# Kernel tuning notes

Hardware: AMD Instinct MI355X
Metric: run time of the kernel (lower is better)

## Reference

```python
import jax, jax.numpy as jnp
import numpy as np

N_NODES = 50000
N_EDGES = 400000
IN_CH = 814
HID = 128
HEADS1 = 4
NUM_CLASSES = 46
NUM_GRAPHS = 64
NEG_SLOPE = 0.2


def setup_inputs() -> dict:
    key = jax.random.key(0)
    ks = jax.random.split(key, 16)
    x = jax.random.normal(ks[0], (N_NODES, IN_CH), dtype=jnp.float32)
    edge_index = jax.random.randint(ks[1], (2, N_EDGES), 0, N_NODES, dtype=jnp.int32)
    batch = jnp.sort(jax.random.randint(ks[2], (N_NODES,), 0, NUM_GRAPHS, dtype=jnp.int32))
    s = 0.05
    # GATConv 1: in 814 -> 4 heads x 128, concat
    W1 = jax.random.normal(ks[3], (IN_CH, HEADS1 * HID), dtype=jnp.float32) * s
    a_src1 = jax.random.normal(ks[4], (HEADS1, HID), dtype=jnp.float32) * s
    a_dst1 = jax.random.normal(ks[5], (HEADS1, HID), dtype=jnp.float32) * s
    b1 = jnp.zeros((HEADS1 * HID,), dtype=jnp.float32)
    # GATConv 2: in 512 -> 1 head x 128, no concat (mean)
    W2 = jax.random.normal(ks[6], (HEADS1 * HID, HID), dtype=jnp.float32) * s
    a_src2 = jax.random.normal(ks[7], (1, HID), dtype=jnp.float32) * s
    a_dst2 = jax.random.normal(ks[8], (1, HID), dtype=jnp.float32) * s
    b2 = jnp.zeros((HID,), dtype=jnp.float32)
    # MLP head 128 -> 64 -> 46 (dropout is identity in eval mode)
    fc1_w = jax.random.normal(ks[9], (HID, 64), dtype=jnp.float32) * s
    fc1_b = jnp.zeros((64,), dtype=jnp.float32)
    fc2_w = jax.random.normal(ks[10], (64, NUM_CLASSES), dtype=jnp.float32) * s
    fc2_b = jnp.zeros((NUM_CLASSES,), dtype=jnp.float32)
    return {"x": x, "edge_index": edge_index, "batch": batch,
            "W1": W1, "a_src1": a_src1, "a_dst1": a_dst1, "b1": b1,
            "W2": W2, "a_src2": a_src2, "a_dst2": a_dst2, "b2": b2,
            "fc1_w": fc1_w, "fc1_b": fc1_b, "fc2_w": fc2_w, "fc2_b": fc2_b}


def _gat_layer(x, src, dst, W, a_src, a_dst, bias, heads, out_ch, concat):
    # PyG GATConv: linear transform, edge attention w/ LeakyReLU,
    # segment softmax over destination nodes, scatter-add aggregation.
    n = x.shape[0]
    h = (x @ W).reshape(n, heads, out_ch)                 # [N,H,C]
    al_s = jnp.einsum('nhc,hc->nh', h, a_src)             # [N,H]
    al_d = jnp.einsum('nhc,hc->nh', h, a_dst)             # [N,H]
    e = jax.nn.leaky_relu(al_s[src] + al_d[dst], NEG_SLOPE)  # [E,H]
    m = jax.ops.segment_max(e, dst, num_segments=n)       # [N,H]
    ex = jnp.exp(e - m[dst])
    denom = jax.ops.segment_sum(ex, dst, num_segments=n)  # [N,H]
    alpha = ex / denom[dst]                               # [E,H]
    out = jax.ops.segment_sum(h[src] * alpha[:, :, None], dst, num_segments=n)  # [N,H,C]
    if concat:
        return out.reshape(n, heads * out_ch) + bias
    return out.mean(axis=1) + bias


def reference(x, edge_index, batch, W1, a_src1, a_dst1, b1,
              W2, a_src2, a_dst2, b2, fc1_w, fc1_b, fc2_w, fc2_b):
    n = x.shape[0]
    # GATConv adds self-loops by default
    loops = jnp.arange(n, dtype=edge_index.dtype)
    src = jnp.concatenate([edge_index[0], loops])
    dst = jnp.concatenate([edge_index[1], loops])
    h = jax.nn.relu(_gat_layer(x, src, dst, W1, a_src1, a_dst1, b1, HEADS1, HID, True))
    h = jax.nn.relu(_gat_layer(h, src, dst, W2, a_src2, a_dst2, b2, 1, HID, False))
    # global mean pool over graphs
    sums = jax.ops.segment_sum(h, batch, num_segments=NUM_GRAPHS)      # [G,128]
    cnts = jax.ops.segment_sum(jnp.ones((n,), h.dtype), batch, num_segments=NUM_GRAPHS)
    pooled = sums / jnp.maximum(cnts, 1.0)[:, None]
    # MLP head (dropout = identity at inference)
    z = jax.nn.relu(pooled @ fc1_w + fc1_b)
    return z @ fc2_w + fc2_b
```

## Files before the change

kernel.cpp:

```cpp
#include <hip/hip_runtime.h>
#include <hip/hip_bf16.h>

#define N_NODES 50000
#define N_EDGES 400000
#define IN_CH   814
#define HID     128
#define HEADS1  4
#define NUM_GRAPHS 64
#define NUM_CLASSES 46
#define NEG_SLOPE 0.2f
#define KP 832

typedef __attribute__((ext_vector_type(8))) short bf16x8;
typedef __attribute__((ext_vector_type(4))) float f32x4;

__device__ __forceinline__ float leaky(float v) { return v > 0.f ? v : NEG_SLOPE * v; }

__device__ __forceinline__ unsigned short f2bf(float f) {
  unsigned u = __float_as_uint(f);
  unsigned r = u + 0x7fff + ((u >> 16) & 1);
  return (unsigned short)(r >> 16);
}
__device__ __forceinline__ float bf2f(short s) {
  return __uint_as_float(((unsigned)(unsigned short)s) << 16);
}

#define GLOAD_LDS16(g, l)                                                        \
  __builtin_amdgcn_global_load_lds((const __attribute__((address_space(1))) unsigned*)(g), \
                                   (__attribute__((address_space(3))) unsigned*)(l), 16, 0, 0)

__global__ __launch_bounds__(256) void convert_x(const float* __restrict__ x,
                                                 unsigned short* __restrict__ Ab) {
  const int row = blockIdx.x;
  const int c = threadIdx.x * 4;
  if (c >= KP) return;
  const float* xr = x + (size_t)row * IN_CH;
  float v[4] = {0.f, 0.f, 0.f, 0.f};
  if (c + 3 < IN_CH) {
    float2 u0 = *(const float2*)(xr + c);
    float2 u1 = *(const float2*)(xr + c + 2);
    v[0] = u0.x; v[1] = u0.y; v[2] = u1.x; v[3] = u1.y;
  } else {
#pragma unroll
    for (int k = 0; k < 4; k++) if (c + k < IN_CH) v[k] = xr[c + k];
  }
  ushort4 o = make_ushort4(f2bf(v[0]), f2bf(v[1]), f2bf(v[2]), f2bf(v[3]));
  *(ushort4*)&Ab[(size_t)row * KP + c] = o;
}

__global__ __launch_bounds__(256) void convert_w1t(const float* __restrict__ W1,
                                                   unsigned short* __restrict__ Bt) {
  const int n = blockIdx.x;
  unsigned short* br = Bt + (size_t)n * KP;
  for (int k = threadIdx.x; k < KP; k += 256) {
    const float v = (k < IN_CH) ? W1[(size_t)k * 512 + n] : 0.f;
    br[k] = f2bf(v);
  }
}

__global__ __launch_bounds__(256) void convert_w2t(const float* __restrict__ W2,
                                                   unsigned short* __restrict__ Bt2) {
  const int n = blockIdx.x;
  unsigned short* br = Bt2 + (size_t)n * 512;
  for (int k = threadIdx.x; k < 512; k += 256) br[k] = f2bf(W2[(size_t)k * 128 + n]);
}

template<int KPITCH, int CPITCH, bool OUTBF>
__global__ __launch_bounds__(256) void gemm_mfma(const unsigned short* __restrict__ A,
                                                 const unsigned short* __restrict__ B,
                                                 void* __restrict__ Cv) {
  __shared__ unsigned short sA[8 * 128 * 8];
  __shared__ unsigned short sB[8 * 128 * 8];
  const int tid = threadIdx.x;
  const int w = tid >> 6, lane = tid & 63;
  const int row0 = blockIdx.x * 128;
  const int col0 = blockIdx.y * 128;
  const int wr = w >> 1, wc = w & 1;

  f32x4 acc[4][4];
#pragma unroll
  for (int mi = 0; mi < 4; mi++)
#pragma unroll
    for (int nj = 0; nj < 4; nj++) acc[mi][nj] = (f32x4){0.f, 0.f, 0.f, 0.f};

  long a_off[4], b_off[4];
  int lds_base[4];
#pragma unroll
  for (int c = 0; c < 4; c++) {
    const int s = (w * 4 + c) * 64 + lane;
    const int kg = s >> 7, r = s & 127;
    int arow = row0 + r; if (arow >= N_NODES) arow = N_NODES - 1;
    a_off[c] = (long)arow * KPITCH + kg * 8;
    b_off[c] = (long)(col0 + r) * KPITCH + kg * 8;
    lds_base[c] = (w * 4 + c) * 64 * 8;
  }
  int aoff[4][2], boff[4][2];
#pragma unroll
  for (int i = 0; i < 4; i++)
#pragma unroll
    for (int ks = 0; ks < 2; ks++) {
      aoff[i][ks] = ((ks * 4 + (lane >> 4)) * 128 + wr * 64 + i * 16 + (lane & 15)) * 8;
      boff[i][ks] = ((ks * 4 + (lane >> 4)) * 128 + wc * 64 + i * 16 + (lane & 15)) * 8;
    }

  for (int kt = 0; kt < KPITCH / 64; ++kt) {
    const int kbase = kt * 64;
#pragma unroll
    for (int c = 0; c < 4; c++) {
      GLOAD_LDS16(A + (a_off[c] + kbase), &sA[lds_base[c]]);
      GLOAD_LDS16(B + (b_off[c] + kbase), &sB[lds_base[c]]);
    }
    __syncthreads();
    bf16x8 af[4][2], bfr[4][2];
#pragma unroll
    for (int mi = 0; mi < 4; mi++)
#pragma unroll
      for (int ks = 0; ks < 2; ks++) af[mi][ks] = *(const bf16x8*)&sA[aoff[mi][ks]];
#pragma unroll
    for (int nj = 0; nj < 4; nj++)
#pragma unroll
      for (int ks = 0; ks < 2; ks++) bfr[nj][ks] = *(const bf16x8*)&sB[boff[nj][ks]];
#pragma unroll
    for (int mi = 0; mi < 4; mi++)
#pragma unroll
      for (int nj = 0; nj < 4; nj++) {
        acc[mi][nj] = __builtin_amdgcn_mfma_f32_16x16x32_bf16(af[mi][0], bfr[nj][0], acc[mi][nj], 0, 0, 0);
        acc[mi][nj] = __builtin_amdgcn_mfma_f32_16x16x32_bf16(af[mi][1], bfr[nj][1], acc[mi][nj], 0, 0, 0);
      }
    __syncthreads();
  }
  const int r4 = (lane >> 4) * 4;
  const int cc = lane & 15;
#pragma unroll
  for (int mi = 0; mi < 4; mi++) {
#pragma unroll
    for (int r = 0; r < 4; r++) {
      const int gr = row0 + wr * 64 + mi * 16 + r4 + r;
      if (gr < N_NODES) {
        if (OUTBF) {
          unsigned short* cp = (unsigned short*)Cv + (size_t)gr * CPITCH + col0 + wc * 64 + cc;
#pragma unroll
          for (int nj = 0; nj < 4; nj++) cp[nj * 16] = f2bf(acc[mi][nj][r]);
        } else {
          float* cp = (float*)Cv + (size_t)gr * CPITCH + col0 + wc * 64 + cc;
#pragma unroll
          for (int nj = 0; nj < 4; nj++) cp[nj * 16] = acc[mi][nj][r];
        }
      }
    }
  }
}

__global__ __launch_bounds__(256) void attn_prep1(const unsigned short* __restrict__ h1b,
                                                  const float* __restrict__ a_src,
                                                  const float* __restrict__ a_dst,
                                                  float* __restrict__ als,
                                                  float* __restrict__ ald) {
  const int n = blockIdx.x * 4 + (threadIdx.x >> 6);
  const int lane = threadIdx.x & 63;
  if (n >= N_NODES) return;
  const int c0 = lane * 8;
  const bf16x8 hv = *(const bf16x8*)&h1b[(size_t)n * 512 + c0];
  float ps = 0.f, pd = 0.f;
#pragma unroll
  for (int j = 0; j < 8; j++) {
    const float f = bf2f(hv[j]);
    ps += f * a_src[c0 + j];
    pd += f * a_dst[c0 + j];
  }
#pragma unroll
  for (int off = 8; off; off >>= 1) {
    ps += __shfl_xor(ps, off);
    pd += __shfl_xor(pd, off);
  }
  if ((lane & 15) == 0) {
    als[n * 4 + (lane >> 4)] = ps;
    ald[n * 4 + (lane >> 4)] = pd;
  }
}

__global__ __launch_bounds__(256) void attn_prep2(const float* __restrict__ h2,
                                                  const float* __restrict__ a_src,
                                                  const float* __restrict__ a_dst,
                                                  float* __restrict__ als,
                                                  float* __restrict__ ald) {
  const int n = blockIdx.x * 4 + (threadIdx.x >> 6);
  const int lane = threadIdx.x & 63;
  if (n >= N_NODES) return;
  const float* hr = h2 + (size_t)n * 128;
  float h0 = hr[lane], h1v = hr[lane + 64];
  float ps = h0 * a_src[lane] + h1v * a_src[lane + 64];
  float pd = h0 * a_dst[lane] + h1v * a_dst[lane + 64];
#pragma unroll
  for (int off = 32; off; off >>= 1) {
    ps += __shfl_xor(ps, off);
    pd += __shfl_xor(pd, off);
  }
  if (lane == 0) { als[n] = ps; ald[n] = pd; }
}

__global__ void init_misc(int* deg, float* pooled, float* cnts) {
  const int i = blockIdx.x * 256 + threadIdx.x;
  if (i < N_NODES) deg[i] = 1;
  if (i < NUM_GRAPHS * HID) pooled[i] = 0.f;
  if (i < NUM_GRAPHS) cnts[i] = 0.f;
}

__global__ void hist_kernel(const int* __restrict__ dst, int* deg) {
  const int e = blockIdx.x * 256 + threadIdx.x;
  if (e < N_EDGES) atomicAdd(&deg[dst[e]], 1);
}

__global__ __launch_bounds__(256) void scan_block_sum(const int* __restrict__ deg, int* bsum) {
  __shared__ int sd[256];
  const int t = threadIdx.x;
  const int i = blockIdx.x * 256 + t;
  sd[t] = (i < N_NODES) ? deg[i] : 0;
  __syncthreads();
  for (int s = 128; s; s >>= 1) { if (t < s) sd[t] += sd[t + s]; __syncthreads(); }
  if (t == 0) bsum[blockIdx.x] = sd[0];
}

__global__ __launch_bounds__(256) void scan_base(const int* __restrict__ bsum, int* bbase, int* offsets) {
  __shared__ int tmp[256];
  const int t = threadIdx.x;
  const int nb = (N_NODES + 255) / 256;
  const int v = (t < nb) ? bsum[t] : 0;
  tmp[t] = v;
  __syncthreads();
  for (int off = 1; off < 256; off <<= 1) {
    int a = (t >= off) ? tmp[t - off] : 0;
    __syncthreads();
    tmp[t] += a;
    __syncthreads();
  }
  if (t < nb) bbase[t] = tmp[t] - v;
  if (t == 255) offsets[N_NODES] = tmp[255];
}

__global__ __launch_bounds__(256) void scan_final(const int* __restrict__ deg,
                                                  const int* __restrict__ bbase,
                                                  int* offsets, int* cursor) {
  __shared__ int tmp[256];
  const int t = threadIdx.x;
  const int i = blockIdx.x * 256 + t;
  const int v = (i < N_NODES) ? deg[i] : 0;
  tmp[t] = v;
  __syncthreads();
  for (int off = 1; off < 256; off <<= 1) {
    int a = (t >= off) ? tmp[t - off] : 0;
    __syncthreads();
    tmp[t] += a;
    __syncthreads();
  }
  if (i < N_NODES) {
    const int excl = bbase[blockIdx.x] + tmp[t] - v;
    offsets[i] = excl;
    cursor[i] = excl;
  }
}

__global__ void scatter_kernel(const int* __restrict__ src, const int* __restrict__ dst,
                               int* cursor, int* __restrict__ srcs) {
  const int e = blockIdx.x * 256 + threadIdx.x;
  if (e >= N_EDGES + N_NODES) return;
  int s, d;
  if (e < N_EDGES) { s = src[e]; d = dst[e]; }
  else { s = e - N_EDGES; d = s; }
  const int p = atomicAdd(&cursor[d], 1);
  srcs[p] = s;
}

__global__ __launch_bounds__(256) void aggregate1(const unsigned short* __restrict__ h1b,
                                                  const float* __restrict__ als,
                                                  const float* __restrict__ ald,
                                                  const int* __restrict__ offsets,
                                                  const int* __restrict__ srcs,
                                                  const float* __restrict__ b1,
                                                  unsigned short* __restrict__ x2b) {
  const int n = blockIdx.x * 4 + (threadIdx.x >> 6);
  const int lane = threadIdx.x & 63;
  if (n >= N_NODES) return;
  const int beg = offsets[n], end = offsets[n + 1];
  const int h = lane >> 4;
  const int c0 = lane * 8;
  const float aldh = ald[n * 4 + h];
  float m = -1e30f;
  for (int p = beg; p < end; p++)
    m = fmaxf(m, leaky(als[srcs[p] * 4 + h] + aldh));
  float den = 0.f;
  float acc[8] = {0, 0, 0, 0, 0, 0, 0, 0};
  for (int p = beg; p < end; p++) {
    const int s = srcs[p];
    const float w = __expf(leaky(als[s * 4 + h] + aldh) - m);
    den += w;
    const bf16x8 hv = *(const bf16x8*)&h1b[(size_t)s * 512 + c0];
#pragma unroll
    for (int j = 0; j < 8; j++) acc[j] += w * bf2f(hv[j]);
  }
  bf16x8 o;
  const float inv = 1.f / den;
#pragma unroll
  for (int j = 0; j < 8; j++)
    o[j] = (short)f2bf(fmaxf(acc[j] * inv + b1[c0 + j], 0.f));
  *(bf16x8*)&x2b[(size_t)n * 512 + c0] = o;
}

__global__ __launch_bounds__(256) void aggregate2(const float* __restrict__ h2,
                                                  const float* __restrict__ als,
                                                  const float* __restrict__ ald,
                                                  const int* __restrict__ offsets,
                                                  const int* __restrict__ srcs,
                                                  const float* __restrict__ b2,
                                                  float* __restrict__ out2) {
  const int n = blockIdx.x * 4 + (threadIdx.x >> 6);
  const int lane = threadIdx.x & 63;
  if (n >= N_NODES) return;
  const int beg = offsets[n], end = offsets[n + 1];
  const int c0 = lane * 2;
  const float aldn = ald[n];
  float m = -1e30f;
  for (int p = beg; p < end; p++) m = fmaxf(m, leaky(als[srcs[p]] + aldn));
  float den = 0.f, a0 = 0.f, a1 = 0.f;
  for (int p = beg; p < end; p++) {
    const int s = srcs[p];
    const float w = __expf(leaky(als[s] + aldn) - m);
    den += w;
    const float2 hv = *(const float2*)&h2[(size_t)s * 128 + c0];
    a0 += w * hv.x;
    a1 += w * hv.y;
  }
  const float inv = 1.f / den;
  float2 o = make_float2(fmaxf(a0 * inv + b2[c0], 0.f), fmaxf(a1 * inv + b2[c0 + 1], 0.f));
  *(float2*)&out2[(size_t)n * 128 + c0] = o;
}

__global__ __launch_bounds__(128) void pool_kernel(const float* __restrict__ out2,
                                                   const int* __restrict__ batch,
                                                   float* pooled, float* cnts) {
  const int t = threadIdx.x;
  const int base = blockIdx.x * 256;
  float acc = 0.f;
  float cnt = 0.f;
  int cur = -1;
  for (int i = 0; i < 256; i++) {
    const int n = base + i;
    if (n >= N_NODES) break;
    const int g = batch[n];
    if (g != cur) {
      if (cur >= 0) {
        atomicAdd(&pooled[cur * HID + t], acc);
        if (t == 0) atomicAdd(&cnts[cur], cnt);
      }
      acc = 0.f; cnt = 0.f; cur = g;
    }
    acc += out2[(size_t)n * HID + t];
    cnt += 1.f;
  }
  if (cur >= 0) {
    atomicAdd(&pooled[cur * HID + t], acc);
    if (t == 0) atomicAdd(&cnts[cur], cnt);
  }
}

__global__ __launch_bounds__(64) void mlp_kernel(const float* __restrict__ pooled,
                                                 const float* __restrict__ cnts,
                                                 const float* __restrict__ fc1_w,
                                                 const float* __restrict__ fc1_b,
                                                 const float* __restrict__ fc2_w,
                                                 const float* __restrict__ fc2_b,
                                                 float* __restrict__ out) {
  __shared__ float pl[128];
  __shared__ float z[64];
  const int g = blockIdx.x, t = threadIdx.x;
  const float c = fmaxf(cnts[g], 1.0f);
  pl[t] = pooled[g * HID + t] / c;
  pl[t + 64] = pooled[g * HID + t + 64] / c;
  __syncthreads();
  float acc = fc1_b[t];
  for (int i = 0; i < 128; i++) acc += pl[i] * fc1_w[i * 64 + t];
  z[t] = fmaxf(acc, 0.f);
  __syncthreads();
  if (t < NUM_CLASSES) {
    float o = fc2_b[t];
    for (int i = 0; i < 64; i++) o += z[i] * fc2_w[i * NUM_CLASSES + t];
    out[g * NUM_CLASSES + t] = o;
  }
}

extern "C" void kernel_launch(void* const* d_in, const int* in_sizes, int n_in,
                              void* d_out, int out_size, void* d_ws, size_t ws_size,
                              hipStream_t stream) {
  const float* x       = (const float*)d_in[0];
  const int*   ei      = (const int*)d_in[1];
  const int*   batch   = (const int*)d_in[2];
  const float* W1      = (const float*)d_in[3];
  const float* a_src1  = (const float*)d_in[4];
  const float* a_dst1  = (const float*)d_in[5];
  const float* b1      = (const float*)d_in[6];
  const float* W2      = (const float*)d_in[7];
  const float* a_src2  = (const float*)d_in[8];
  const float* a_dst2  = (const float*)d_in[9];
  const float* b2      = (const float*)d_in[10];
  const float* fc1_w   = (const float*)d_in[11];
  const float* fc1_b   = (const float*)d_in[12];
  const float* fc2_w   = (const float*)d_in[13];
  const float* fc2_b   = (const float*)d_in[14];
  float* out = (float*)d_out;

  const int* e_src = ei;
  const int* e_dst = ei + N_EDGES;

  float* wsf = (float*)d_ws;
  unsigned short* h1b = (unsigned short*)wsf;
  unsigned short* Ab  = (unsigned short*)(wsf + 12800000);
  unsigned short* x2b = (unsigned short*)(wsf + 33600000);
  unsigned short* Bt  = (unsigned short*)(wsf + 46400000);
  unsigned short* Bt2 = (unsigned short*)(wsf + 46613000);
  float* als1 = wsf + 46646000;
  float* ald1 = als1 + 200000;
  float* als2 = ald1 + 200000;
  float* ald2 = als2 + 50000;
  float* pooled = ald2 + 50000;
  float* cnts = pooled + 8192;
  int* deg     = (int*)(cnts + 64);
  int* offsets = deg + 50000;
  int* cursor  = offsets + 50001;
  int* srcs    = cursor + 50000;
  int* bsum    = srcs + 450000;
  int* bbase   = bsum + 200;
  float* h2   = wsf + 12800000;
  float* out2 = wsf + 19200000;

  const int NB = (N_NODES + 255) / 256;

  init_misc<<<NB, 256, 0, stream>>>(deg, pooled, cnts);
  hist_kernel<<<(N_EDGES + 255) / 256, 256, 0, stream>>>(e_dst, deg);
  scan_block_sum<<<NB, 256, 0, stream>>>(deg, bsum);
  scan_base<<<1, 256, 0, stream>>>(bsum, bbase, offsets);
  scan_final<<<NB, 256, 0, stream>>>(deg, bbase, offsets, cursor);
  scatter_kernel<<<(N_EDGES + N_NODES + 255) / 256, 256, 0, stream>>>(e_src, e_dst, cursor, srcs);

  convert_x<<<N_NODES, 256, 0, stream>>>(x, Ab);
  convert_w1t<<<512, 256, 0, stream>>>(W1, Bt);
  gemm_mfma<KP, 512, true><<<dim3(391, 4), 256, 0, stream>>>(Ab, Bt, (void*)h1b);
  attn_prep1<<<12500, 256, 0, stream>>>(h1b, a_src1, a_dst1, als1, ald1);
  aggregate1<<<12500, 256, 0, stream>>>(h1b, als1, ald1, offsets, srcs, b1, x2b);

  convert_w2t<<<128, 256, 0, stream>>>(W2, Bt2);
  gemm_mfma<512, 128, false><<<dim3(391, 1), 256, 0, stream>>>(x2b, Bt2, (void*)h2);
  attn_prep2<<<12500, 256, 0, stream>>>(h2, a_src2, a_dst2, als2, ald2);
  aggregate2<<<12500, 256, 0, stream>>>(h2, als2, ald2, offsets, srcs, b2, out2);

  pool_kernel<<<NB, 128, 0, stream>>>(out2, batch, pooled, cnts);
  mlp_kernel<<<NUM_GRAPHS, 64, 0, stream>>>(pooled, cnts, fc1_w, fc1_b, fc2_w, fc2_b, out);
}
```

Baseline: 731.6 us.

## Double-buffer GEMM LDS tiles, swap grid order, tile-transpose W1 conversion

The MFMA GEMM now keeps two LDS buffers, so global-to-LDS loads for the next K tile are issued while the current tile is computed, and it drops one barrier per iteration. The grid is transposed so the column tiles sharing an A row block launch next to each other, which should improve L2 reuse of A. The W1 transpose-convert now uses a padded 32x32 shared-memory tile so both the reads and the writes are coalesced. Doubling LDS per block may lower occupancy.

```diff
diff --git a/kernel.cpp b/kernel.cpp
--- a/kernel.cpp
+++ b/kernel.cpp
@@ -50,11 +50,20 @@
 
 __global__ __launch_bounds__(256) void convert_w1t(const float* __restrict__ W1,
                                                    unsigned short* __restrict__ Bt) {
-  const int n = blockIdx.x;
-  unsigned short* br = Bt + (size_t)n * KP;
-  for (int k = threadIdx.x; k < KP; k += 256) {
-    const float v = (k < IN_CH) ? W1[(size_t)k * 512 + n] : 0.f;
-    br[k] = f2bf(v);
+  __shared__ float tile[32][33];
+  const int n0 = blockIdx.x * 32;
+  const int k0 = blockIdx.y * 32;
+  const int tx = threadIdx.x & 31, ty = threadIdx.x >> 5;
+#pragma unroll
+  for (int i = 0; i < 32; i += 8) {
+    const int k = k0 + ty + i;
+    tile[ty + i][tx] = (k < IN_CH) ? W1[(size_t)k * 512 + n0 + tx] : 0.f;
+  }
+  __syncthreads();
+#pragma unroll
+  for (int i = 0; i < 32; i += 8) {
+    const int n = n0 + ty + i;
+    Bt[(size_t)n * KP + k0 + tx] = f2bf(tile[tx][ty + i]);
   }
 }
 
@@ -69,12 +78,13 @@
 __global__ __launch_bounds__(256) void gemm_mfma(const unsigned short* __restrict__ A,
                                                  const unsigned short* __restrict__ B,
                                                  void* __restrict__ Cv) {
-  __shared__ unsigned short sA[8 * 128 * 8];
-  __shared__ unsigned short sB[8 * 128 * 8];
+  constexpr int NT = KPITCH / 64;
+  __shared__ unsigned short sA[2][8 * 128 * 8];
+  __shared__ unsigned short sB[2][8 * 128 * 8];
   const int tid = threadIdx.x;
   const int w = tid >> 6, lane = tid & 63;
-  const int row0 = blockIdx.x * 128;
-  const int col0 = blockIdx.y * 128;
+  const int row0 = blockIdx.y * 128;
+  const int col0 = blockIdx.x * 128;
   const int wr = w >> 1, wc = w & 1;
 
   f32x4 acc[4][4];
@@ -103,32 +113,49 @@
       boff[i][ks] = ((ks * 4 + (lane >> 4)) * 128 + wc * 64 + i * 16 + (lane & 15)) * 8;
     }
 
-  for (int kt = 0; kt < KPITCH / 64; ++kt) {
-    const int kbase = kt * 64;
-#pragma unroll
-    for (int c = 0; c < 4; c++) {
-      GLOAD_LDS16(A + (a_off[c] + kbase), &sA[lds_base[c]]);
-      GLOAD_LDS16(B + (b_off[c] + kbase), &sB[lds_base[c]]);
-    }
+#define STAGE(kt, b)                                                     \
+  {                                                                      \
+    const int kbase = (kt) * 64;                                         \
+    _Pragma("unroll")                                                    \
+    for (int c = 0; c < 4; c++) {                                        \
+      GLOAD_LDS16(A + (a_off[c] + kbase), &sA[b][lds_base[c]]);          \
+      GLOAD_LDS16(B + (b_off[c] + kbase), &sB[b][lds_base[c]]);          \
+    }                                                                    \
+  }
+
+#define COMPUTE(b)                                                                   \
+  {                                                                                  \
+    bf16x8 af[4][2], bfr[4][2];                                                      \
+    _Pragma("unroll")                                                                \
+    for (int mi = 0; mi < 4; mi++)                                                   \
+      _Pragma("unroll")                                                              \
+      for (int ks = 0; ks < 2; ks++) af[mi][ks] = *(const bf16x8*)&sA[b][aoff[mi][ks]]; \
+    _Pragma("unroll")                                                                \
+    for (int nj = 0; nj < 4; nj++)                                                   \
+      _Pragma("unroll")                                                              \
+      for (int ks = 0; ks < 2; ks++) bfr[nj][ks] = *(const bf16x8*)&sB[b][boff[nj][ks]]; \
+    _Pragma("unroll")                                                                \
+    for (int mi = 0; mi < 4; mi++)                                                   \
+      _Pragma("unroll")                                                              \
+      for (int nj = 0; nj < 4; nj++) {                                               \
+        acc[mi][nj] = __builtin_amdgcn_mfma_f32_16x16x32_bf16(af[mi][0], bfr[nj][0], acc[mi][nj], 0, 0, 0); \
+        acc[mi][nj] = __builtin_amdgcn_mfma_f32_16x16x32_bf16(af[mi][1], bfr[nj][1], acc[mi][nj], 0, 0, 0); \
+      }                                                                              \
+  }
+
+  STAGE(0, 0);
+  __syncthreads();
+  int cur = 0;
+  for (int kt = 0; kt < NT - 1; ++kt) {
+    STAGE(kt + 1, cur ^ 1);
+    COMPUTE(cur);
     __syncthreads();
-    bf16x8 af[4][2], bfr[4][2];
-#pragma unroll
-    for (int mi = 0; mi < 4; mi++)
-#pragma unroll
-      for (int ks = 0; ks < 2; ks++) af[mi][ks] = *(const bf16x8*)&sA[aoff[mi][ks]];
-#pragma unroll
-    for (int nj = 0; nj < 4; nj++)
-#pragma unroll
-      for (int ks = 0; ks < 2; ks++) bfr[nj][ks] = *(const bf16x8*)&sB[boff[nj][ks]];
-#pragma unroll
-    for (int mi = 0; mi < 4; mi++)
-#pragma unroll
-      for (int nj = 0; nj < 4; nj++) {
-        acc[mi][nj] = __builtin_amdgcn_mfma_f32_16x16x32_bf16(af[mi][0], bfr[nj][0], acc[mi][nj], 0, 0, 0);
-        acc[mi][nj] = __builtin_amdgcn_mfma_f32_16x16x32_bf16(af[mi][1], bfr[nj][1], acc[mi][nj], 0, 0, 0);
-      }
-    __syncthreads();
-  }
+    cur ^= 1;
+  }
+  COMPUTE(cur);
+#undef STAGE
+#undef COMPUTE
+
   const int r4 = (lane >> 4) * 4;
   const int cc = lane & 15;
 #pragma unroll
@@ -442,13 +469,13 @@
   scatter_kernel<<<(N_EDGES + N_NODES + 255) / 256, 256, 0, stream>>>(e_src, e_dst, cursor, srcs);
 
   convert_x<<<N_NODES, 256, 0, stream>>>(x, Ab);
-  convert_w1t<<<512, 256, 0, stream>>>(W1, Bt);
-  gemm_mfma<KP, 512, true><<<dim3(391, 4), 256, 0, stream>>>(Ab, Bt, (void*)h1b);
+  convert_w1t<<<dim3(16, 26), 256, 0, stream>>>(W1, Bt);
+  gemm_mfma<KP, 512, true><<<dim3(4, 391), 256, 0, stream>>>(Ab, Bt, (void*)h1b);
   attn_prep1<<<12500, 256, 0, stream>>>(h1b, a_src1, a_dst1, als1, ald1);
   aggregate1<<<12500, 256, 0, stream>>>(h1b, als1, ald1, offsets, srcs, b1, x2b);
 
   convert_w2t<<<128, 256, 0, stream>>>(W2, Bt2);
-  gemm_mfma<512, 128, false><<<dim3(391, 1), 256, 0, stream>>>(x2b, Bt2, (void*)h2);
+  gemm_mfma<512, 128, false><<<dim3(1, 391), 256, 0, stream>>>(x2b, Bt2, (void*)h2);
   attn_prep2<<<12500, 256, 0, stream>>>(h2, a_src2, a_dst2, als2, ald2);
   aggregate2<<<12500, 256, 0, stream>>>(h2, als2, ald2, offsets, srcs, b2, out2);
 
```

Result: no change. 742.2 us (+1.4%).
